# Kernel tuning notes

Hardware: AMD Instinct MI355X
Metric: run time of the kernel (lower is better)

The kernel has to match this reference:

```python
import jax, jax.numpy as jnp
import numpy as np
from jax import lax

NQ = 5  # qubits
NL = 3  # circuit layers


def conv2d(x, w, b):
    y = lax.conv_general_dilated(x, w, (1, 1), 'SAME',
                                 dimension_numbers=('NCHW', 'OIHW', 'NCHW'))
    return y + b[None, :, None, None]


def batchnorm(x, g, b, eps=1e-5):
    # training-mode batch statistics over (N,H,W), matching nn.BatchNorm2d in train()
    mu = x.mean((0, 2, 3), keepdims=True)
    var = x.var((0, 2, 3), keepdims=True)
    return g[None, :, None, None] * (x - mu) * lax.rsqrt(var + eps) + b[None, :, None, None]


def maxpool2(x):
    return lax.reduce_window(x, -jnp.inf, lax.max, (1, 1, 2, 2), (1, 1, 2, 2), 'VALID')


def _apply_1q(state, U, w):
    # state: (2,)*NQ, wire w is axis w (PennyLane default.qubit ordering)
    s = jnp.tensordot(U, state, axes=([1], [w]))
    return jnp.moveaxis(s, 0, w)


def _cnot(state, c, t):
    s0 = jnp.take(state, 0, axis=c)
    s1 = jnp.take(state, 1, axis=c)
    ta = t if t < c else t - 1
    s1 = jnp.flip(s1, axis=ta)  # X on target when control=1
    return jnp.stack([s0, s1], axis=c)


def _rx(t):
    c, s = jnp.cos(t / 2), jnp.sin(t / 2)
    return jnp.array([[c, -1j * s], [-1j * s, c]], dtype=jnp.complex64)


def _ry(t):
    c, s = jnp.cos(t / 2), jnp.sin(t / 2)
    return jnp.array([[c, -s], [s, c]], dtype=jnp.complex64)


def _rz(t):
    e = jnp.exp(-1j * t / 2)
    z = jnp.zeros((), jnp.complex64)
    return jnp.array([[e, z], [z, jnp.conj(e)]], dtype=jnp.complex64)


def quantum_circuit(inputs, weights):
    # inputs: (5,), weights: (30,)  -> scalar <Z0 Z1 Z2>
    state = jnp.zeros((2,) * NQ, jnp.complex64).at[(0,) * NQ].set(1.0)
    npl = NQ * 2  # weights per layer = 10
    nw = weights.shape[0]
    for l in range(NL):
        for i in range(NQ):
            state = _apply_1q(state, _rx(inputs[i]), i)
        for i in range(NQ):
            state = _apply_1q(state, _ry(weights[(l * npl + i) % nw]), i)
            state = _apply_1q(state, _rz(weights[(l * npl + i + NQ) % nw]), i)
        for i in range(NQ - 1):
            state = _cnot(state, i, i + 1)
        state = _cnot(state, NQ - 1, 0)
    probs = jnp.abs(state) ** 2
    z = jnp.array([1.0, -1.0], jnp.float32)
    sign = z[:, None, None] * z[None, :, None] * z[None, None, :]  # Z on wires 0,1,2
    return jnp.sum(probs * sign[:, :, :, None, None])


def setup_inputs() -> dict:
    key = jax.random.key(0)
    ks = jax.random.split(key, 12)
    d = {}
    d['x'] = jax.random.normal(ks[0], (256, 1, 224, 224), jnp.float32)
    d['conv1_w'] = jax.random.normal(ks[1], (16, 1, 3, 3), jnp.float32) * 0.1
    d['conv1_b'] = jnp.zeros((16,), jnp.float32)
    d['bn1_g'] = jnp.ones((16,), jnp.float32)
    d['bn1_b'] = jnp.zeros((16,), jnp.float32)
    d['conv2_w'] = jax.random.normal(ks[2], (32, 16, 3, 3), jnp.float32) * 0.05
    d['conv2_b'] = jnp.zeros((32,), jnp.float32)
    d['bn2_g'] = jnp.ones((32,), jnp.float32)
    d['bn2_b'] = jnp.zeros((32,), jnp.float32)
    d['conv3_w'] = jax.random.normal(ks[3], (64, 32, 3, 3), jnp.float32) * 0.05
    d['conv3_b'] = jnp.zeros((64,), jnp.float32)
    d['bn3_g'] = jnp.ones((64,), jnp.float32)
    d['bn3_b'] = jnp.zeros((64,), jnp.float32)
    d['fc1_w'] = jax.random.normal(ks[4], (64, 5), jnp.float32) * 0.1   # (in,out)
    d['fc1_b'] = jnp.zeros((5,), jnp.float32)
    d['ln_g'] = jnp.ones((5,), jnp.float32)
    d['ln_b'] = jnp.zeros((5,), jnp.float32)
    d['q_params'] = jax.random.uniform(ks[5], (30,), jnp.float32)
    d['fc2_w'] = jax.random.normal(ks[6], (1, 32), jnp.float32) * 0.5
    d['fc2_b'] = jnp.zeros((32,), jnp.float32)
    d['fc3_w'] = jax.random.normal(ks[7], (32, 2), jnp.float32) * 0.2
    d['fc3_b'] = jnp.zeros((2,), jnp.float32)
    return d


def reference(x, conv1_w, conv1_b, bn1_g, bn1_b, conv2_w, conv2_b, bn2_g, bn2_b,
              conv3_w, conv3_b, bn3_g, bn3_b, fc1_w, fc1_b, ln_g, ln_b,
              q_params, fc2_w, fc2_b, fc3_w, fc3_b):
    h = maxpool2(jax.nn.relu(batchnorm(conv2d(x, conv1_w, conv1_b), bn1_g, bn1_b)))
    h = maxpool2(jax.nn.relu(batchnorm(conv2d(h, conv2_w, conv2_b), bn2_g, bn2_b)))
    h = maxpool2(jax.nn.relu(batchnorm(conv2d(h, conv3_w, conv3_b), bn3_g, bn3_b)))
    # dropout is identity in eval; adaptive avg pool (1,1) + flatten
    h = h.mean((2, 3))                    # (B, 64)
    h = h @ fc1_w + fc1_b                 # (B, 5)
    mu = h.mean(-1, keepdims=True)
    var = h.var(-1, keepdims=True)
    h = ln_g * (h - mu) * lax.rsqrt(var + 1e-5) + ln_b
    q = jax.vmap(lambda inp: quantum_circuit(inp, q_params))(h)  # (B,)
    q = q[:, None].astype(jnp.float32)    # (B, 1)
    h2 = jax.nn.relu(q @ fc2_w + fc2_b)   # (B, 32)
    logits = h2 @ fc3_w + fc3_b           # (B, 2)
    return jax.nn.log_softmax(logits, axis=1)
```

## Files before the change

### kernel.cpp

```cpp
#include <hip/hip_runtime.h>
#include <hip/hip_bf16.h>


typedef _Float16 f16;
typedef _Float16 f16x2 __attribute__((ext_vector_type(2)));
typedef _Float16 f16x4 __attribute__((ext_vector_type(4)));
typedef _Float16 f16x8 __attribute__((ext_vector_type(8)));
typedef float f32x4 __attribute__((ext_vector_type(4)));
typedef float f32x16 __attribute__((ext_vector_type(16)));

#define DEV static __device__ __forceinline__

DEV float wave_sum(float v) {
#pragma unroll
  for (int off = 32; off > 0; off >>= 1) v += __shfl_xor(v, off, 64);
  return v;
}

__global__ __launch_bounds__(256) void repack(const float* __restrict__ w2,
                                              const float* __restrict__ w3,
                                              f16* __restrict__ Bt2,
                                              f16* __restrict__ Bt3) {
  int t = blockIdx.x * 256 + threadIdx.x;
  int T = gridDim.x * 256;
  for (int i = t; i < 32 * 168; i += T) {
    int oc = i / 168, kk = i - oc * 168;
    float v = 0.f;
    if (kk < 144) {
      int tap = kk >> 4, ic = kk & 15;
      v = w2[(oc * 16 + ic) * 9 + tap];
    }
    Bt2[i] = (f16)v;
  }
  for (int i = t; i < 64 * 296; i += T) {
    int oc = i / 296, kk = i - oc * 296;
    float v = 0.f;
    if (kk < 288) {
      int tap = kk / 32, ic = kk & 31;
      v = w3[(oc * 32 + ic) * 9 + tap];
    }
    Bt3[i] = (f16)v;
  }
}

__global__ __launch_bounds__(64) void finalize(const float* __restrict__ banks,
                                               const float* __restrict__ g,
                                               const float* __restrict__ b,
                                               float* __restrict__ scsh, int C,
                                               float inv_n) {
  int c = blockIdx.x, bk = threadIdx.x;
  float s = banks[bk * 2 * C + c];
  float qq = banks[bk * 2 * C + C + c];
  s = wave_sum(s);
  qq = wave_sum(qq);
  if (bk == 0) {
    float mean = s * inv_n;
    float var = qq * inv_n - mean * mean;
    float sc = g[c] * rsqrtf(var + 1e-5f);
    scsh[c] = sc;
    scsh[C + c] = b[c] - mean * sc;
  }
}

__global__ __launch_bounds__(256) void l1_mfma32(const float* __restrict__ x,
                                                 const float* __restrict__ w1,
                                                 float* __restrict__ banks,
                                                 f16* __restrict__ h1raw) {
  __shared__ f16 xA[18 * 240];
  __shared__ f16 xB[18 * 240];
  __shared__ f16 lrow[4 * 3616];
  __shared__ float lstat[32];
  int bid = blockIdx.x;
  int n = bid / 14, band = bid - n * 14;
  int y0 = band * 16;
  int t = threadIdx.x;
  if (t < 32) lstat[t] = 0.f;
  for (int i = t; i < 1008; i += 256) {
    int r = i / 56, k = i - r * 56;
    int y = y0 - 1 + r;
    float4 v = make_float4(0.f, 0.f, 0.f, 0.f);
    if ((unsigned)y < 224u)
      v = *(const float4*)(x + ((size_t)(n * 224 + y)) * 224 + k * 4);
    f16 h0 = (f16)v.x, h1 = (f16)v.y, h2 = (f16)v.z, h3 = (f16)v.w;
    f16* pa = xA + r * 240 + 4 * k + 1;
    pa[0] = h0; pa[1] = h1; pa[2] = h2; pa[3] = h3;
    f16x4 pk = {h0, h1, h2, h3};
    *(f16x4*)(xB + r * 240 + 4 * k) = pk;
  }
  if (t < 18) {
    xA[t * 240 + 0] = (f16)0.f;
    xA[t * 240 + 225] = (f16)0.f;
    xA[t * 240 + 226] = (f16)0.f;
    xB[t * 240 + 224] = (f16)0.f;
    xB[t * 240 + 225] = (f16)0.f;
  }
  __syncthreads();

  int wave = t >> 6, lane = t & 63;
  int g = lane >> 5, m32 = lane & 31;
  int oc = m32 & 15, s = m32 >> 4;

  f16x8 b;
#pragma unroll
  for (int j = 0; j < 8; j++) {
    int ky = 2 * g + (j >> 2), kx = j & 3;
    int kys = ky - s;
    float wv = 0.f;
    if (kx < 3 && kys >= 0 && kys < 3) wv = w1[oc * 9 + kys * 3 + kx];
    b[j] = (f16)wv;
  }

  const f16* abase = (m32 & 1) ? (xB + (m32 - 1)) : (xA + m32);
  f16* myrow = lrow + wave * 3616;
  f16* mrow = myrow + s * 1808;
  f32x16 zero16;
#pragma unroll
  for (int r = 0; r < 16; r++) zero16[r] = 0.f;
  const int bp[8] = {0, 1, 4, 5, 8, 9, 12, 13};
  float ssum = 0.f, ssq = 0.f;

  for (int rp = wave; rp < 8; rp += 4) {
    int r0 = 2 * rp + 2 * g;
    const f16* rbase = abase + r0 * 240;
#pragma unroll
    for (int xt = 0; xt < 7; xt++) {
      const f16* p0 = rbase + xt * 32;
      f16x2 v0 = *(const f16x2*)(p0);
      f16x2 v1 = *(const f16x2*)(p0 + 2);
      f16x2 v2 = *(const f16x2*)(p0 + 240);
      f16x2 v3 = *(const f16x2*)(p0 + 242);
      f16x8 a = {v0[0], v0[1], v1[0], v1[1], v2[0], v2[1], v3[0], v3[1]};
      f32x16 acc = __builtin_amdgcn_mfma_f32_32x32x16_f16(a, b, zero16, 0, 0, 0);
#pragma unroll
      for (int r = 0; r < 16; r++) {
        float v = acc[r];
        ssum += v;
        ssq += v * v;
      }
#pragma unroll
      for (int i = 0; i < 8; i++) {
        float pm = fmaxf(acc[2 * i], acc[2 * i + 1]);
        int pxp = xt * 16 + bp[i] + 2 * g;
        mrow[pxp * 16 + oc] = (f16)pm;
      }
    }
    int ph = band * 8 + rp;
    f16* gdst = h1raw + ((size_t)(n * 112) + ph) * 112 * 16;
    for (int i = lane; i < 224; i += 64) {
      f16x8 va = *(const f16x8*)(myrow + i * 8);
      f16x8 vb = *(const f16x8*)(myrow + 1808 + i * 8);
#pragma unroll
      for (int k = 0; k < 8; k++) va[k] = (va[k] > vb[k]) ? va[k] : vb[k];
      *(f16x8*)(gdst + i * 8) = va;
    }
  }
  ssum += __shfl_xor(ssum, 16, 64);
  ssum += __shfl_xor(ssum, 32, 64);
  ssq += __shfl_xor(ssq, 16, 64);
  ssq += __shfl_xor(ssq, 32, 64);
  if (lane < 16) {
    atomicAdd(&lstat[oc], ssum);
    atomicAdd(&lstat[16 + oc], ssq);
  }
  __syncthreads();
  if (t < 32) atomicAdd(&banks[(bid & 63) * 32 + t], lstat[t]);
}

__global__ __launch_bounds__(256, 2) void l2_gemm(
    const f16* __restrict__ h1, const f16* __restrict__ Btg,
    const float* __restrict__ scsh1, f16* __restrict__ p2,
    float* __restrict__ banks) {
  extern __shared__ char smem[];
  f16* lin0 = (f16*)smem;
  f16* lin1 = (f16*)(smem + 32832);
  f16* lpool = (f16*)(smem + 65664);
  float* lstat = (float*)(smem + 72832);
  int bid = blockIdx.x;
  int n = bid / 7, sb = bid - n * 7;
  int t = threadIdx.x;
  int wave = t >> 6, lane = t & 63, q = lane >> 4, wi = lane & 15;
  const int icq = (q & 1) * 8;

  f16x8 breg0[5], breg1[5];
#pragma unroll
  for (int j = 0; j < 5; j++) {
    breg0[j] = *(const f16x8*)(Btg + wi * 168 + j * 32 + q * 8);
    breg1[j] = *(const f16x8*)(Btg + (16 + wi) * 168 + j * 32 + q * 8);
  }

  f16x8 L[6];
  {
    int gb4 = sb * 16;
#pragma unroll
    for (int k = 0; k < 6; k++) {
      int i = t + k * 256;
      f16x8 v = {0, 0, 0, 0, 0, 0, 0, 0};
      if (i < 1344) {
        int r = i / 224, c = i - r * 224;
        int y = gb4 + r - 1;
        if ((unsigned)y < 112u)
          v = *(const f16x8*)(h1 + ((size_t)(n * 112 + y)) * 112 * 16 + c * 8);
      }
      L[k] = v;
    }
  }
  __builtin_amdgcn_sched_barrier(0);
  if (t < 64) lstat[t] = 0.f;
  if (t < 48) {
    f16* dst = (t < 24) ? lin0 : lin1;
    int tt = (t < 24) ? t : t - 24;
    int r = tt >> 2, k2 = tt & 3;
    f16x8 z = {0, 0, 0, 0, 0, 0, 0, 0};
    int pos = (k2 < 2) ? 0 : 113;
    *(f16x8*)(dst + (r * 114 + pos) * 24 + (k2 & 1) * 8) = z;
  }
  {
    int gb4 = sb * 16;
#pragma unroll
    for (int k = 0; k < 6; k++) {
      int i = t + k * 256;
      if (i < 1344) {
        int r = i / 224, c = i - r * 224;
        int y = gb4 + r - 1;
        f16x8 o = {0, 0, 0, 0, 0, 0, 0, 0};
        if ((unsigned)y < 112u) {
          f16x8 xv = L[k];
          int ch0 = (c & 1) * 8;
#pragma unroll
          for (int e = 0; e < 8; e++) {
            float f = (float)xv[e] * scsh1[ch0 + e] + scsh1[16 + ch0 + e];
            o[e] = (f16)fmaxf(f, 0.f);
          }
        }
        *(f16x8*)(lin0 + (r * 114 + 1 + (c >> 1)) * 24 + (c & 1) * 8) = o;
      }
    }
  }
  __syncthreads();

  float tS0 = 0.f, tQ0 = 0.f, tS1 = 0.f, tQ1 = 0.f;
  f16* cur = lin0;
  f16* nxt = lin1;

  for (int b = 0; b < 4; b++) {
    int gb = sb * 4 + b;
    if (b < 3) {
      int gb4 = (gb + 1) * 4;
#pragma unroll
      for (int k = 0; k < 6; k++) {
        int i = t + k * 256;
        f16x8 v = {0, 0, 0, 0, 0, 0, 0, 0};
        if (i < 1344) {
          int r = i / 224, c = i - r * 224;
          int y = gb4 + r - 1;
          if ((unsigned)y < 112u)
            v = *(const f16x8*)(h1 +
                                ((size_t)(n * 112 + y)) * 112 * 16 + c * 8);
        }
        L[k] = v;
      }
      __builtin_amdgcn_sched_barrier(0);
    }

    f32x4 acc[7][2];
#pragma unroll
    for (int f = 0; f < 7; f++)
#pragma unroll
      for (int nf = 0; nf < 2; nf++)
#pragma unroll
        for (int r = 0; r < 4; r++) acc[f][nf][r] = 0.f;

#pragma unroll
    for (int j = 0; j < 5; j++) {
      const int tA = 2 * j, tB = 2 * j + 1;
      const int kyA = tA / 3, kxA = tA % 3;
      const int kyB = (tB < 9) ? tB / 3 : 0, kxB = (tB < 9) ? tB % 3 : 0;
      bool hiq = (q >= 2);
      int ky = hiq ? kyB : kyA;
      int kx = hiq ? kxB : kxA;
      const f16* aptr0 = cur + ((wave + ky) * 114 + wi + kx) * 24 + icq;
      f16x8 b0 = breg0[j];
      f16x8 b1 = breg1[j];
#pragma unroll
      for (int f = 0; f < 7; f++) {
        f16x8 a = *(const f16x8*)(aptr0 + f * 384);
        acc[f][0] =
            __builtin_amdgcn_mfma_f32_16x16x32_f16(a, b0, acc[f][0], 0, 0, 0);
        acc[f][1] =
            __builtin_amdgcn_mfma_f32_16x16x32_f16(a, b1, acc[f][1], 0, 0, 0);
      }
    }

#pragma unroll
    for (int f = 0; f < 7; f++)
#pragma unroll
      for (int r = 0; r < 4; r++) {
        float v0 = acc[f][0][r], v1 = acc[f][1][r];
        tS0 += v0; tQ0 += v0 * v0;
        tS1 += v1; tQ1 += v1 * v1;
      }

    if (wave & 1) {
#pragma unroll
      for (int f = 0; f < 7; f++)
#pragma unroll
        for (int nf = 0; nf < 2; nf++) {
          int ch = nf * 16 + wi;
          int pc0 = f * 8 + q * 2;
          float m0 = fmaxf(acc[f][nf][0], acc[f][nf][1]);
          float m1 = fmaxf(acc[f][nf][2], acc[f][nf][3]);
          lpool[((wave >> 1) * 56 + pc0) * 32 + ch] = (f16)m0;
          lpool[((wave >> 1) * 56 + pc0 + 1) * 32 + ch] = (f16)m1;
        }
    }

    if (b < 3) {
      int gb4 = (gb + 1) * 4;
#pragma unroll
      for (int k = 0; k < 6; k++) {
        int i = t + k * 256;
        if (i < 1344) {
          int r = i / 224, c = i - r * 224;
          int y = gb4 + r - 1;
          f16x8 o = {0, 0, 0, 0, 0, 0, 0, 0};
          if ((unsigned)y < 112u) {
            f16x8 xv = L[k];
            int ch0 = (c & 1) * 8;
#pragma unroll
            for (int e = 0; e < 8; e++) {
              float f = (float)xv[e] * scsh1[ch0 + e] + scsh1[16 + ch0 + e];
              o[e] = (f16)fmaxf(f, 0.f);
            }
          }
          *(f16x8*)(nxt + (r * 114 + 1 + (c >> 1)) * 24 + (c & 1) * 8) = o;
        }
      }
    }
    __syncthreads();

    if (!(wave & 1)) {
      int ph = gb * 2 + (wave >> 1);
#pragma unroll
      for (int f = 0; f < 7; f++)
#pragma unroll
        for (int nf = 0; nf < 2; nf++) {
          int ch = nf * 16 + wi;
          int pc0 = f * 8 + q * 2;
          float m0 = fmaxf(acc[f][nf][0], acc[f][nf][1]);
          float m1 = fmaxf(acc[f][nf][2], acc[f][nf][3]);
          m0 = fmaxf(m0, (float)lpool[((wave >> 1) * 56 + pc0) * 32 + ch]);
          m1 = fmaxf(m1, (float)lpool[((wave >> 1) * 56 + pc0 + 1) * 32 + ch]);
          size_t ob = (((size_t)n * 56 + ph) * 56) * 32;
          p2[ob + (size_t)pc0 * 32 + ch] = (f16)m0;
          p2[ob + (size_t)(pc0 + 1) * 32 + ch] = (f16)m1;
        }
    }
    __syncthreads();

    f16* tmpp = cur; cur = nxt; nxt = tmpp;
  }

  tS0 += __shfl_xor(tS0, 16, 64); tS0 += __shfl_xor(tS0, 32, 64);
  tQ0 += __shfl_xor(tQ0, 16, 64); tQ0 += __shfl_xor(tQ0, 32, 64);
  tS1 += __shfl_xor(tS1, 16, 64); tS1 += __shfl_xor(tS1, 32, 64);
  tQ1 += __shfl_xor(tQ1, 16, 64); tQ1 += __shfl_xor(tQ1, 32, 64);
  if (q == 0) {
    atomicAdd(&lstat[wi], tS0);
    atomicAdd(&lstat[16 + wi], tS1);
    atomicAdd(&lstat[32 + wi], tQ0);
    atomicAdd(&lstat[48 + wi], tQ1);
  }
  __syncthreads();
  if (t < 64) {
    int i = t >> 5, c = t & 31;
    atomicAdd(&banks[(bid & 63) * 64 + i * 32 + c], lstat[i * 32 + c]);
  }
}

__global__ __launch_bounds__(256, 2) void l3_gemm(
    const f16* __restrict__ p2, const f16* __restrict__ Btg,
    const float* __restrict__ scsh2, f16* __restrict__ p3,
    float* __restrict__ banks) {
  extern __shared__ char smem[];
  f16* lin = (f16*)smem;
  float* lstat = (float*)(smem + 46400);
  f16* lpool = (f16*)smem;
  int bx = blockIdx.x;
  int n = bx / 7, sb = bx - n * 7;
  int t = threadIdx.x;
  int wave = t >> 6, lane = t & 63, q = lane >> 4, wi = lane & 15;

  f16x8 breg[9][4];
#pragma unroll
  for (int j = 0; j < 9; j++)
#pragma unroll
    for (int h = 0; h < 4; h++)
      breg[j][h] =
          *(const f16x8*)(Btg + (h * 16 + wi) * 296 + j * 32 + q * 8);

  if (t < 128) lstat[t] = 0.f;
#pragma unroll
  for (int k = 0; k < 9; k++) {
    int i = t + k * 256;
    if (i < 2240) {
      int r = i / 224, rem = i - r * 224;
      int c = rem >> 2, cp = rem & 3;
      int y = sb * 8 + r - 1;
      f16x8 o = {0, 0, 0, 0, 0, 0, 0, 0};
      if ((unsigned)y < 56u) {
        f16x8 xv =
            *(const f16x8*)(p2 + (((size_t)(n * 56 + y)) * 56 + c) * 32 +
                            cp * 8);
        int ch0 = cp * 8;
#pragma unroll
        for (int e = 0; e < 8; e++) {
          float f = (float)xv[e] * scsh2[ch0 + e] + scsh2[32 + ch0 + e];
          o[e] = (f16)fmaxf(f, 0.f);
        }
      }
      *(f16x8*)(lin + (r * 58 + 1 + c) * 40 + cp * 8) = o;
    }
  }
  if (t < 80) {
    int r = t / 8, k = t & 7;
    int col = (k < 4) ? 0 : 57, cp = k & 3;
    f16x8 z = {0, 0, 0, 0, 0, 0, 0, 0};
    *(f16x8*)(lin + (r * 58 + col) * 40 + cp * 8) = z;
  }
  __syncthreads();

  int abase[7];
#pragma unroll
  for (int f = 0; f < 7; f++) {
    int pos = wave * 112 + f * 16 + wi;
    int r = pos / 56, w = pos - r * 56;
    abase[f] = (r * 58 + w) * 40 + q * 8;
  }
  f32x4 acc[7][4];
#pragma unroll
  for (int f = 0; f < 7; f++)
#pragma unroll
    for (int h = 0; h < 4; h++)
#pragma unroll
      for (int r = 0; r < 4; r++) acc[f][h][r] = 0.f;

#pragma unroll
  for (int j = 0; j < 9; j++) {
    const int ky = j / 3, kx = j % 3;
#pragma unroll
    for (int f = 0; f < 7; f++) {
      f16x8 a = *(const f16x8*)(lin + abase[f] + (ky * 58 + kx) * 40);
#pragma unroll
      for (int h = 0; h < 4; h++)
        acc[f][h] =
            __builtin_amdgcn_mfma_f32_16x16x32_f16(a, breg[j][h], acc[f][h],
                                                   0, 0, 0);
    }
  }

  float tS[4] = {0.f, 0.f, 0.f, 0.f}, tQ[4] = {0.f, 0.f, 0.f, 0.f};
#pragma unroll
  for (int f = 0; f < 7; f++)
#pragma unroll
    for (int h = 0; h < 4; h++)
#pragma unroll
      for (int r = 0; r < 4; r++) {
        float v = acc[f][h][r];
        tS[h] += v;
        tQ[h] += v * v;
      }
#pragma unroll
  for (int h = 0; h < 4; h++) {
    tS[h] += __shfl_xor(tS[h], 16, 64); tS[h] += __shfl_xor(tS[h], 32, 64);
    tQ[h] += __shfl_xor(tQ[h], 16, 64); tQ[h] += __shfl_xor(tQ[h], 32, 64);
  }
  if (q == 0) {
#pragma unroll
    for (int h = 0; h < 4; h++) {
      atomicAdd(&lstat[h * 16 + wi], tS[h]);
      atomicAdd(&lstat[64 + h * 16 + wi], tQ[h]);
    }
  }
  __syncthreads();

#pragma unroll
  for (int f = 0; f < 7; f++) {
    int pos = wave * 112 + f * 16 + q * 4;
    int r0 = pos / 56, w0 = pos - r0 * 56;
#pragma unroll
    for (int h = 0; h < 4; h++) {
      int ch = h * 16 + wi;
      float m0 = fmaxf(acc[f][h][0], acc[f][h][1]);
      float m1 = fmaxf(acc[f][h][2], acc[f][h][3]);
      lpool[(r0 * 28 + (w0 >> 1)) * 64 + ch] = (f16)m0;
      lpool[(r0 * 28 + (w0 >> 1) + 1) * 64 + ch] = (f16)m1;
    }
  }
  __syncthreads();

  for (int i = t; i < 7168; i += 256) {
    int ch = i & 63, rest = i >> 6;
    int pc = rest % 28, pr = rest / 28;
    float v = fmaxf((float)lpool[((2 * pr) * 28 + pc) * 64 + ch],
                    (float)lpool[((2 * pr + 1) * 28 + pc) * 64 + ch]);
    int gpr = sb * 4 + pr;
    p3[(((size_t)n * 28 + gpr) * 28 + pc) * 64 + ch] = (f16)v;
  }
  if (t < 128) {
    atomicAdd(&banks[(bx & 63) * 128 + t], lstat[t]);
  }
}

__global__ __launch_bounds__(256) void head_pool(
    const f16* __restrict__ p3, const float* __restrict__ scsh3,
    const float* __restrict__ fc1w, const float* __restrict__ fc1b,
    float* __restrict__ featg) {
  int n = blockIdx.x, t = threadIdx.x;
  __shared__ float red[64 * 33];
  __shared__ float meanc[64];
  int oct = t & 7, strip = t >> 3;
  float sc[8], sh[8];
#pragma unroll
  for (int k = 0; k < 8; k++) {
    sc[k] = scsh3[oct * 8 + k];
    sh[k] = scsh3[64 + oct * 8 + k];
  }
  float acc[8];
#pragma unroll
  for (int k = 0; k < 8; k++) acc[k] = 0.f;
  const f16* base = p3 + (size_t)n * 50176 + oct * 8;
  for (int px = strip; px < 784; px += 32) {
    f16x8 v = *(const f16x8*)(base + (size_t)px * 64);
#pragma unroll
    for (int k = 0; k < 8; k++)
      acc[k] += fmaxf((float)v[k] * sc[k] + sh[k], 0.f);
  }
#pragma unroll
  for (int k = 0; k < 8; k++) red[(oct * 8 + k) * 33 + strip] = acc[k];
  __syncthreads();
  if (t < 64) {
    float s = 0.f;
    for (int j = 0; j < 32; j++) s += red[t * 33 + j];
    meanc[t] = s * (1.f / 784.f);
  }
  __syncthreads();
  if (t < 5) {
    float a = fc1b[t];
    for (int i = 0; i < 64; i++) a += meanc[i] * fc1w[i * 5 + t];
    featg[n * 8 + t] = a;
  }
}

template <int W>
DEV void g_rx(float (&sr)[32], float (&si)[32], float c, float s) {
  constexpr int m = 1 << (4 - W);
#pragma unroll
  for (int i0 = 0; i0 < 32; i0++)
    if (!(i0 & m)) {
      int i1 = i0 | m;
      float a0r = sr[i0], a0i = si[i0], a1r = sr[i1], a1i = si[i1];
      sr[i0] = c * a0r + s * a1i;
      si[i0] = c * a0i - s * a1r;
      sr[i1] = s * a0i + c * a1r;
      si[i1] = -s * a0r + c * a1i;
    }
}

template <int W>
DEV void g_ry(float (&sr)[32], float (&si)[32], float c, float s) {
  constexpr int m = 1 << (4 - W);
#pragma unroll
  for (int i0 = 0; i0 < 32; i0++)
    if (!(i0 & m)) {
      int i1 = i0 | m;
      float a0r = sr[i0], a0i = si[i0], a1r = sr[i1], a1i = si[i1];
      sr[i0] = c * a0r - s * a1r;
      si[i0] = c * a0i - s * a1i;
      sr[i1] = s * a0r + c * a1r;
      si[i1] = s * a0i + c * a1i;
    }
}

template <int W>
DEV void g_rz(float (&sr)[32], float (&si)[32], float c, float s) {
  constexpr int m = 1 << (4 - W);
#pragma unroll
  for (int i0 = 0; i0 < 32; i0++)
    if (!(i0 & m)) {
      int i1 = i0 | m;
      float a0r = sr[i0], a0i = si[i0], a1r = sr[i1], a1i = si[i1];
      sr[i0] = c * a0r + s * a0i;
      si[i0] = c * a0i - s * a0r;
      sr[i1] = c * a1r - s * a1i;
      si[i1] = c * a1i + s * a1r;
    }
}

template <int C, int T>
DEV void g_cnot(float (&sr)[32], float (&si)[32]) {
  constexpr int mc = 1 << (4 - C), mt = 1 << (4 - T);
#pragma unroll
  for (int i0 = 0; i0 < 32; i0++)
    if ((i0 & mc) && !(i0 & mt)) {
      int i1 = i0 | mt;
      float tr = sr[i0]; sr[i0] = sr[i1]; sr[i1] = tr;
      float ti = si[i0]; si[i0] = si[i1]; si[i1] = ti;
    }
}

__global__ __launch_bounds__(64) void head_q(
    const float* __restrict__ featg, const float* __restrict__ lng,
    const float* __restrict__ lnb, const float* __restrict__ qp,
    const float* __restrict__ fc2w, const float* __restrict__ fc2b,
    const float* __restrict__ fc3w, const float* __restrict__ fc3b,
    float* __restrict__ out) {
  int n = blockIdx.x * 64 + threadIdx.x;
  float f[5];
#pragma unroll
  for (int i = 0; i < 5; i++) f[i] = featg[n * 8 + i];
  float mu = (f[0] + f[1] + f[2] + f[3] + f[4]) * 0.2f;
  float var = 0.f;
#pragma unroll
  for (int i = 0; i < 5; i++) { float d = f[i] - mu; var += d * d; }
  var *= 0.2f;
  float inv = rsqrtf(var + 1e-5f);
#pragma unroll
  for (int i = 0; i < 5; i++) f[i] = lng[i] * (f[i] - mu) * inv + lnb[i];

  float cx[5], sx[5];
#pragma unroll
  for (int i = 0; i < 5; i++) {
    cx[i] = cosf(0.5f * f[i]);
    sx[i] = sinf(0.5f * f[i]);
  }
  float sr[32], si[32];
#pragma unroll
  for (int i = 0; i < 32; i++) { sr[i] = 0.f; si[i] = 0.f; }
  sr[0] = 1.f;

  for (int l = 0; l < 3; l++) {
    g_rx<0>(sr, si, cx[0], sx[0]);
    g_rx<1>(sr, si, cx[1], sx[1]);
    g_rx<2>(sr, si, cx[2], sx[2]);
    g_rx<3>(sr, si, cx[3], sx[3]);
    g_rx<4>(sr, si, cx[4], sx[4]);
#define WIRE_YZ(I)                                             \
  {                                                            \
    float ty = qp[l * 10 + I];                                 \
    g_ry<I>(sr, si, cosf(0.5f * ty), sinf(0.5f * ty));         \
    float tz = qp[l * 10 + I + 5];                             \
    g_rz<I>(sr, si, cosf(0.5f * tz), sinf(0.5f * tz));         \
  }
    WIRE_YZ(0) WIRE_YZ(1) WIRE_YZ(2) WIRE_YZ(3) WIRE_YZ(4)
#undef WIRE_YZ
    g_cnot<0, 1>(sr, si);
    g_cnot<1, 2>(sr, si);
    g_cnot<2, 3>(sr, si);
    g_cnot<3, 4>(sr, si);
    g_cnot<4, 0>(sr, si);
  }
  float qv = 0.f;
#pragma unroll
  for (int idx = 0; idx < 32; idx++) {
    float p = sr[idx] * sr[idx] + si[idx] * si[idx];
    qv += (__popc(idx & 0x1C) & 1) ? -p : p;
  }
  float l0 = fc3b[0], l1 = fc3b[1];
  for (int j = 0; j < 32; j++) {
    float hv = fmaxf(qv * fc2w[j] + fc2b[j], 0.f);
    l0 += hv * fc3w[j * 2];
    l1 += hv * fc3w[j * 2 + 1];
  }
  float mx = fmaxf(l0, l1);
  float lse = mx + logf(expf(l0 - mx) + expf(l1 - mx));
  out[n * 2 + 0] = l0 - lse;
  out[n * 2 + 1] = l1 - lse;
}

extern "C" void kernel_launch(void* const* d_in, const int* in_sizes, int n_in,
                              void* d_out, int out_size, void* d_ws,
                              size_t ws_size, hipStream_t stream) {
  const float* x    = (const float*)d_in[0];
  const float* w1   = (const float*)d_in[1];
  const float* bn1g = (const float*)d_in[3];
  const float* bn1b = (const float*)d_in[4];
  const float* w2   = (const float*)d_in[5];
  const float* bn2g = (const float*)d_in[7];
  const float* bn2b = (const float*)d_in[8];
  const float* w3   = (const float*)d_in[9];
  const float* bn3g = (const float*)d_in[11];
  const float* bn3b = (const float*)d_in[12];
  const float* fc1w = (const float*)d_in[13];
  const float* fc1b = (const float*)d_in[14];
  const float* lng  = (const float*)d_in[15];
  const float* lnb  = (const float*)d_in[16];
  const float* qp   = (const float*)d_in[17];
  const float* fc2w = (const float*)d_in[18];
  const float* fc2b = (const float*)d_in[19];
  const float* fc3w = (const float*)d_in[20];
  const float* fc3b = (const float*)d_in[21];
  float* out = (float*)d_out;

  char* ws = (char*)d_ws;
  float* banks1 = (float*)ws;
  float* banks2 = (float*)(ws + 8192);
  float* banks3 = (float*)(ws + 24576);
  float* scsh1 = (float*)(ws + 57344);
  float* scsh2 = (float*)(ws + 57472);
  float* scsh3 = (float*)(ws + 57728);
  f16* Bt2 = (f16*)(ws + 58240);
  f16* Bt3 = (f16*)(ws + 68992);
  f16* h1 = (f16*)(ws + 106880);
  f16* p2 = (f16*)(ws + 106880 + 102760448ULL);
  f16* p3 = (f16*)(ws + 106880 + 102760448ULL + 51380224ULL);
  float* featg = banks2;

  hipMemsetAsync(ws, 0, 57344, stream);
  repack<<<16, 256, 0, stream>>>(w2, w3, Bt2, Bt3);
  l1_mfma32<<<3584, 256, 0, stream>>>(x, w1, banks1, h1);
  finalize<<<16, 64, 0, stream>>>(banks1, bn1g, bn1b, scsh1, 16,
                                  1.f / 12845056.f);
  l2_gemm<<<1792, 256, 73088, stream>>>(h1, Bt2, scsh1, p2, banks2);
  finalize<<<32, 64, 0, stream>>>(banks2, bn2g, bn2b, scsh2, 32,
                                  1.f / 3211264.f);
  l3_gemm<<<1792, 256, 46912, stream>>>(p2, Bt3, scsh2, p3, banks3);
  finalize<<<64, 64, 0, stream>>>(banks3, bn3g, bn3b, scsh3, 64,
                                  1.f / 802816.f);
  head_pool<<<256, 256, 0, stream>>>(p3, scsh3, fc1w, fc1b, featg);
  head_q<<<4, 64, 0, stream>>>(featg, lng, lnb, qp, fc2w, fc2b, fc3w, fc3b,
                               out);
}
```

Before: 351.7 us.

## Restructure conv2 kernel to one-shot 8-row tiles with in-register pooling

The l2_gemm kernel stops looping over four double-buffered 4-row bands per block and instead loads a single 10-row halo tile, so each wave computes two adjacent conv rows. That lets the 2x2 max pool finish in registers, removing the shared-memory pool exchange and the per-band barriers. The grid doubles to 3584 blocks and shared memory per block drops. In exchange the explicit global-load/compute overlap is gone, halo reload overhead rises from 6/4 to 10/8 rows, and accumulator register pressure doubles, which could limit occupancy.

```diff
diff --git a/kernel.cpp b/kernel.cpp
--- a/kernel.cpp
+++ b/kernel.cpp
@@ -171,12 +171,10 @@
     const float* __restrict__ scsh1, f16* __restrict__ p2,
     float* __restrict__ banks) {
   extern __shared__ char smem[];
-  f16* lin0 = (f16*)smem;
-  f16* lin1 = (f16*)(smem + 32832);
-  f16* lpool = (f16*)(smem + 65664);
-  float* lstat = (float*)(smem + 72832);
+  f16* lin = (f16*)smem;
+  float* lstat = (float*)(smem + 54720);
   int bid = blockIdx.x;
-  int n = bid / 7, sb = bid - n * 7;
+  int n = bid / 14, sb = bid - n * 14;
   int t = threadIdx.x;
   int wave = t >> 6, lane = t & 63, q = lane >> 4, wi = lane & 15;
   const int icq = (q & 1) * 8;
@@ -188,176 +186,98 @@
     breg1[j] = *(const f16x8*)(Btg + (16 + wi) * 168 + j * 32 + q * 8);
   }
 
-  f16x8 L[6];
-  {
-    int gb4 = sb * 16;
-#pragma unroll
-    for (int k = 0; k < 6; k++) {
-      int i = t + k * 256;
-      f16x8 v = {0, 0, 0, 0, 0, 0, 0, 0};
-      if (i < 1344) {
-        int r = i / 224, c = i - r * 224;
-        int y = gb4 + r - 1;
-        if ((unsigned)y < 112u)
-          v = *(const f16x8*)(h1 + ((size_t)(n * 112 + y)) * 112 * 16 + c * 8);
-      }
-      L[k] = v;
-    }
-  }
-  __builtin_amdgcn_sched_barrier(0);
   if (t < 64) lstat[t] = 0.f;
-  if (t < 48) {
-    f16* dst = (t < 24) ? lin0 : lin1;
-    int tt = (t < 24) ? t : t - 24;
-    int r = tt >> 2, k2 = tt & 3;
+#pragma unroll
+  for (int k = 0; k < 9; k++) {
+    int i = t + k * 256;
+    if (i < 2240) {
+      int r = i / 224, c = i - r * 224;
+      int y = sb * 8 + r - 1;
+      f16x8 o = {0, 0, 0, 0, 0, 0, 0, 0};
+      if ((unsigned)y < 112u) {
+        f16x8 xv =
+            *(const f16x8*)(h1 + ((size_t)(n * 112 + y)) * 112 * 16 + c * 8);
+        int ch0 = (c & 1) * 8;
+#pragma unroll
+        for (int e = 0; e < 8; e++) {
+          float f = (float)xv[e] * scsh1[ch0 + e] + scsh1[16 + ch0 + e];
+          o[e] = (f16)fmaxf(f, 0.f);
+        }
+      }
+      *(f16x8*)(lin + (r * 114 + 1 + (c >> 1)) * 24 + (c & 1) * 8) = o;
+    }
+  }
+  if (t < 40) {
+    int r = t >> 2, k2 = t & 3;
     f16x8 z = {0, 0, 0, 0, 0, 0, 0, 0};
     int pos = (k2 < 2) ? 0 : 113;
-    *(f16x8*)(dst + (r * 114 + pos) * 24 + (k2 & 1) * 8) = z;
-  }
-  {
-    int gb4 = sb * 16;
-#pragma unroll
-    for (int k = 0; k < 6; k++) {
-      int i = t + k * 256;
-      if (i < 1344) {
-        int r = i / 224, c = i - r * 224;
-        int y = gb4 + r - 1;
-        f16x8 o = {0, 0, 0, 0, 0, 0, 0, 0};
-        if ((unsigned)y < 112u) {
-          f16x8 xv = L[k];
-          int ch0 = (c & 1) * 8;
-#pragma unroll
-          for (int e = 0; e < 8; e++) {
-            float f = (float)xv[e] * scsh1[ch0 + e] + scsh1[16 + ch0 + e];
-            o[e] = (f16)fmaxf(f, 0.f);
-          }
-        }
-        *(f16x8*)(lin0 + (r * 114 + 1 + (c >> 1)) * 24 + (c & 1) * 8) = o;
-      }
-    }
-  }
-  __syncthreads();
-
-  float tS0 = 0.f, tQ0 = 0.f, tS1 = 0.f, tQ1 = 0.f;
-  f16* cur = lin0;
-  f16* nxt = lin1;
-
-  for (int b = 0; b < 4; b++) {
-    int gb = sb * 4 + b;
-    if (b < 3) {
-      int gb4 = (gb + 1) * 4;
-#pragma unroll
-      for (int k = 0; k < 6; k++) {
-        int i = t + k * 256;
-        f16x8 v = {0, 0, 0, 0, 0, 0, 0, 0};
-        if (i < 1344) {
-          int r = i / 224, c = i - r * 224;
-          int y = gb4 + r - 1;
-          if ((unsigned)y < 112u)
-            v = *(const f16x8*)(h1 +
-                                ((size_t)(n * 112 + y)) * 112 * 16 + c * 8);
-        }
-        L[k] = v;
-      }
-      __builtin_amdgcn_sched_barrier(0);
-    }
-
-    f32x4 acc[7][2];
+    *(f16x8*)(lin + (r * 114 + pos) * 24 + (k2 & 1) * 8) = z;
+  }
+  __syncthreads();
+
+  f32x4 acc[2][7][2];
+#pragma unroll
+  for (int rr = 0; rr < 2; rr++)
 #pragma unroll
     for (int f = 0; f < 7; f++)
 #pragma unroll
       for (int nf = 0; nf < 2; nf++)
 #pragma unroll
-        for (int r = 0; r < 4; r++) acc[f][nf][r] = 0.f;
-
-#pragma unroll
-    for (int j = 0; j < 5; j++) {
-      const int tA = 2 * j, tB = 2 * j + 1;
-      const int kyA = tA / 3, kxA = tA % 3;
-      const int kyB = (tB < 9) ? tB / 3 : 0, kxB = (tB < 9) ? tB % 3 : 0;
-      bool hiq = (q >= 2);
-      int ky = hiq ? kyB : kyA;
-      int kx = hiq ? kxB : kxA;
-      const f16* aptr0 = cur + ((wave + ky) * 114 + wi + kx) * 24 + icq;
-      f16x8 b0 = breg0[j];
-      f16x8 b1 = breg1[j];
+        for (int r = 0; r < 4; r++) acc[rr][f][nf][r] = 0.f;
+
+#pragma unroll
+  for (int j = 0; j < 5; j++) {
+    const int tA = 2 * j, tB = 2 * j + 1;
+    const int kyA = tA / 3, kxA = tA % 3;
+    const int kyB = (tB < 9) ? tB / 3 : 0, kxB = (tB < 9) ? tB % 3 : 0;
+    bool hiq = (q >= 2);
+    int ky = hiq ? kyB : kyA;
+    int kx = hiq ? kxB : kxA;
+    f16x8 b0 = breg0[j];
+    f16x8 b1 = breg1[j];
+#pragma unroll
+    for (int rr = 0; rr < 2; rr++) {
+      int ro = 2 * wave + rr;
+      const f16* aptr0 = lin + ((ro + ky) * 114 + wi + kx) * 24 + icq;
 #pragma unroll
       for (int f = 0; f < 7; f++) {
         f16x8 a = *(const f16x8*)(aptr0 + f * 384);
-        acc[f][0] =
-            __builtin_amdgcn_mfma_f32_16x16x32_f16(a, b0, acc[f][0], 0, 0, 0);
-        acc[f][1] =
-            __builtin_amdgcn_mfma_f32_16x16x32_f16(a, b1, acc[f][1], 0, 0, 0);
-      }
-    }
-
+        acc[rr][f][0] =
+            __builtin_amdgcn_mfma_f32_16x16x32_f16(a, b0, acc[rr][f][0], 0, 0, 0);
+        acc[rr][f][1] =
+            __builtin_amdgcn_mfma_f32_16x16x32_f16(a, b1, acc[rr][f][1], 0, 0, 0);
+      }
+    }
+  }
+
+  float tS0 = 0.f, tQ0 = 0.f, tS1 = 0.f, tQ1 = 0.f;
+#pragma unroll
+  for (int rr = 0; rr < 2; rr++)
 #pragma unroll
     for (int f = 0; f < 7; f++)
 #pragma unroll
       for (int r = 0; r < 4; r++) {
-        float v0 = acc[f][0][r], v1 = acc[f][1][r];
+        float v0 = acc[rr][f][0][r], v1 = acc[rr][f][1][r];
         tS0 += v0; tQ0 += v0 * v0;
         tS1 += v1; tQ1 += v1 * v1;
       }
 
-    if (wave & 1) {
-#pragma unroll
-      for (int f = 0; f < 7; f++)
-#pragma unroll
-        for (int nf = 0; nf < 2; nf++) {
-          int ch = nf * 16 + wi;
-          int pc0 = f * 8 + q * 2;
-          float m0 = fmaxf(acc[f][nf][0], acc[f][nf][1]);
-          float m1 = fmaxf(acc[f][nf][2], acc[f][nf][3]);
-          lpool[((wave >> 1) * 56 + pc0) * 32 + ch] = (f16)m0;
-          lpool[((wave >> 1) * 56 + pc0 + 1) * 32 + ch] = (f16)m1;
-        }
-    }
-
-    if (b < 3) {
-      int gb4 = (gb + 1) * 4;
-#pragma unroll
-      for (int k = 0; k < 6; k++) {
-        int i = t + k * 256;
-        if (i < 1344) {
-          int r = i / 224, c = i - r * 224;
-          int y = gb4 + r - 1;
-          f16x8 o = {0, 0, 0, 0, 0, 0, 0, 0};
-          if ((unsigned)y < 112u) {
-            f16x8 xv = L[k];
-            int ch0 = (c & 1) * 8;
-#pragma unroll
-            for (int e = 0; e < 8; e++) {
-              float f = (float)xv[e] * scsh1[ch0 + e] + scsh1[16 + ch0 + e];
-              o[e] = (f16)fmaxf(f, 0.f);
-            }
-          }
-          *(f16x8*)(nxt + (r * 114 + 1 + (c >> 1)) * 24 + (c & 1) * 8) = o;
-        }
-      }
-    }
-    __syncthreads();
-
-    if (!(wave & 1)) {
-      int ph = gb * 2 + (wave >> 1);
-#pragma unroll
-      for (int f = 0; f < 7; f++)
-#pragma unroll
-        for (int nf = 0; nf < 2; nf++) {
-          int ch = nf * 16 + wi;
-          int pc0 = f * 8 + q * 2;
-          float m0 = fmaxf(acc[f][nf][0], acc[f][nf][1]);
-          float m1 = fmaxf(acc[f][nf][2], acc[f][nf][3]);
-          m0 = fmaxf(m0, (float)lpool[((wave >> 1) * 56 + pc0) * 32 + ch]);
-          m1 = fmaxf(m1, (float)lpool[((wave >> 1) * 56 + pc0 + 1) * 32 + ch]);
-          size_t ob = (((size_t)n * 56 + ph) * 56) * 32;
-          p2[ob + (size_t)pc0 * 32 + ch] = (f16)m0;
-          p2[ob + (size_t)(pc0 + 1) * 32 + ch] = (f16)m1;
-        }
-    }
-    __syncthreads();
-
-    f16* tmpp = cur; cur = nxt; nxt = tmpp;
+  {
+    int ph = sb * 4 + wave;
+    size_t ob = (((size_t)n * 56 + ph) * 56) * 32;
+#pragma unroll
+    for (int f = 0; f < 7; f++)
+#pragma unroll
+      for (int nf = 0; nf < 2; nf++) {
+        int ch = nf * 16 + wi;
+        int pc0 = f * 8 + q * 2;
+        float a0 = fmaxf(acc[0][f][nf][0], acc[0][f][nf][1]);
+        float a1 = fmaxf(acc[0][f][nf][2], acc[0][f][nf][3]);
+        float b0m = fmaxf(acc[1][f][nf][0], acc[1][f][nf][1]);
+        float b1m = fmaxf(acc[1][f][nf][2], acc[1][f][nf][3]);
+        p2[ob + (size_t)pc0 * 32 + ch] = (f16)fmaxf(a0, b0m);
+        p2[ob + (size_t)(pc0 + 1) * 32 + ch] = (f16)fmaxf(a1, b1m);
+      }
   }
 
   tS0 += __shfl_xor(tS0, 16, 64); tS0 += __shfl_xor(tS0, 32, 64);
@@ -720,7 +640,7 @@
   l1_mfma32<<<3584, 256, 0, stream>>>(x, w1, banks1, h1);
   finalize<<<16, 64, 0, stream>>>(banks1, bn1g, bn1b, scsh1, 16,
                                   1.f / 12845056.f);
-  l2_gemm<<<1792, 256, 73088, stream>>>(h1, Bt2, scsh1, p2, banks2);
+  l2_gemm<<<3584, 256, 54976, stream>>>(h1, Bt2, scsh1, p2, banks2);
   finalize<<<32, 64, 0, stream>>>(banks2, bn2g, bn2b, scsh2, 32,
                                   1.f / 3211264.f);
   l3_gemm<<<1792, 256, 46912, stream>>>(p2, Bt3, scsh2, p3, banks3);
```

Result: no change. 350.0 us (-0.5%).
